# Optimization experiments

Hardware: AMD Instinct MI355X
Metric: run time of the kernel (lower is better)

Reference implementation:

```python
import jax, jax.numpy as jnp
import numpy as np

D_MODEL = 1024
H = 16
D_HEAD = D_MODEL // H  # 64


def setup_inputs() -> dict:
    key = jax.random.key(0)
    ks = jax.random.split(key, 11)
    B, L = 4, 1024
    s = 0.02
    return {
        "Q": jax.random.normal(ks[0], (B, L, D_MODEL), jnp.float32),
        "K": jax.random.normal(ks[1], (B, L, D_MODEL), jnp.float32),
        "V": jax.random.normal(ks[2], (B, L, D_MODEL), jnp.float32),
        # per-head Dense weights stacked on a leading head axis (Keras Dense: y = x @ W + b)
        "Wq": jax.random.normal(ks[3], (H, D_MODEL, D_HEAD), jnp.float32) * s,
        "bq": jnp.zeros((H, D_HEAD), jnp.float32),
        "Wk": jax.random.normal(ks[4], (H, D_MODEL, D_HEAD), jnp.float32) * s,
        "bk": jnp.zeros((H, D_HEAD), jnp.float32),
        "Wv": jax.random.normal(ks[5], (H, D_MODEL, D_HEAD), jnp.float32) * s,
        "bv": jnp.zeros((H, D_HEAD), jnp.float32),
        "Wo": jax.random.normal(ks[6], (D_MODEL, D_MODEL), jnp.float32) * s,
        "bo": jnp.zeros((D_MODEL,), jnp.float32),
    }


def reference(Q, K, V, Wq, bq, Wk, bk, Wv, bv, Wo, bo):
    # per-head projections, vectorized over heads: [B, H, L, Dh]
    q = jnp.einsum("bld,hde->bhle", Q, Wq) + bq[None, :, None, :]
    k = jnp.einsum("bld,hde->bhle", K, Wk) + bk[None, :, None, :]
    v = jnp.einsum("bld,hde->bhle", V, Wv) + bv[None, :, None, :]
    # scaled dot-product attention scores: [B, H, Lq, Lk]
    scores = jnp.einsum("bhqe,bhke->bhqk", q, k) / jnp.sqrt(jnp.asarray(D_HEAD, q.dtype))
    attn = jax.nn.softmax(scores, axis=-1)
    out_h = jnp.einsum("bhqk,bhke->bhqe", attn, v)  # [B, H, Lq, Dh]
    # concat heads along feature dim (matches tf.concat(heads, axis=2))
    B, Hh, Lq, Dh = out_h.shape
    concat = out_h.transpose(0, 2, 1, 3).reshape(B, Lq, Hh * Dh)
    output = concat @ Wo + bo
    # tf.stack(heads_attention) -> [H, B, Lq, Lk]
    attention = attn.transpose(1, 0, 2, 3)
    return output, attention
```

## Files before the change

### kernel.cpp

```cpp
#include <hip/hip_runtime.h>
#include <stdint.h>

#define DEVI __device__ __forceinline__
typedef unsigned short u16;
typedef __attribute__((ext_vector_type(8))) short s16x8;
typedef __attribute__((ext_vector_type(4))) float f32x4;

typedef __attribute__((address_space(1))) void as1_void;
typedef __attribute__((address_space(3))) void as3_void;

DEVI u16 f2b(float f){
  union { float f; uint32_t u; } x; x.f = f;
  return (u16)((x.u + 0x7fffu + ((x.u >> 16) & 1u)) >> 16);
}

DEVI void gload16(const void* g, void* l){
  __builtin_amdgcn_global_load_lds((as1_void*)g, (as3_void*)l, 16, 0, 0);
}

DEVI f32x4 MFMA(s16x8 a, s16x8 b, f32x4 c){
  return __builtin_amdgcn_mfma_f32_16x16x32_bf16(a, b, c, 0, 0, 0);
}

__global__ __launch_bounds__(256)
void k_prep(const float* __restrict__ Q, const float* __restrict__ Kc,
            const float* __restrict__ V,
            u16* __restrict__ Qb, u16* __restrict__ Kb, u16* __restrict__ Vb,
            const float* __restrict__ Wq, const float* __restrict__ Wk,
            const float* __restrict__ Wv, const float* __restrict__ Wo,
            u16* __restrict__ WqT, u16* __restrict__ WkT,
            u16* __restrict__ WvT, u16* __restrict__ WoT){
  __shared__ float t[64][65];
  const int bid = blockIdx.x, tid = threadIdx.x;
  if(bid < 12288){
    int tno = bid >> 12;
    int blk = bid & 4095;
    const float* s = (tno == 0) ? Q : (tno == 1) ? Kc : V;
    u16* d = (tno == 0) ? Qb : (tno == 1) ? Kb : Vb;
    int i = (blk * 256 + tid) * 4;
    float4 v = *(const float4*)(s + i);
    ushort4 o;
    o.x = f2b(v.x); o.y = f2b(v.y); o.z = f2b(v.z); o.w = f2b(v.w);
    *(ushort4*)(d + i) = o;
  } else {
    int j = bid - 12288;
    const float* src; u16* dst; int C, r0, c0;
    const int R = 1024;
    if(j < 768){
      int tno = j >> 8, rem = j & 255;
      int head = rem >> 4, rt = rem & 15;
      src = ((tno == 0) ? Wq : (tno == 1) ? Wk : Wv) + head * 65536;
      dst = ((tno == 0) ? WqT : (tno == 1) ? WkT : WvT) + head * 65536;
      C = 64; r0 = rt * 64; c0 = 0;
    } else {
      int j2 = j - 768;
      src = Wo; dst = WoT; C = 1024;
      r0 = (j2 & 15) * 64; c0 = (j2 >> 4) * 64;
    }
    int tx = tid & 63, ty = tid >> 6;
    #pragma unroll
    for(int i = 0; i < 64; i += 4)
      t[ty + i][tx] = src[(size_t)(r0 + ty + i) * C + c0 + tx];
    __syncthreads();
    #pragma unroll
    for(int i = 0; i < 64; i += 4)
      dst[(size_t)(c0 + ty + i) * R + r0 + tx] = f2b(t[tx][ty + i]);
  }
}

template<int BM>
DEVI void gemm_core(int mode, const u16* __restrict__ A, const u16* __restrict__ Bt,
                    const float* __restrict__ bias, void* __restrict__ Cp,
                    int m0, int n0, u16* sAb, u16* sBb){
  const int tid = threadIdx.x, w = tid >> 6, l = tid & 63;
  const int wr = w >> 1, wc = w & 1;
  constexpr int MI = BM / 32;
  f32x4 acc[MI][4];
  #pragma unroll
  for(int a = 0; a < MI; a++)
    #pragma unroll
    for(int b = 0; b < 4; b++) acc[a][b] = (f32x4){0.f, 0.f, 0.f, 0.f};

  const int NT = 16;
  auto STAGE = [&](int buf, int t){
    #pragma unroll
    for(int s2 = 0; s2 < BM / 32; s2++){
      int s = (BM / 32) * w + s2;
      int r = s * 8 + (l >> 3);
      int ch = (l & 7) ^ (r & 7);
      gload16((const char*)A + ((size_t)(m0 + r) * 1024 + t * 64) * 2 + ch * 16,
              (char*)(sAb + (size_t)buf * BM * 64) + s * 1024 + l * 16);
    }
    #pragma unroll
    for(int s2 = 0; s2 < 4; s2++){
      int s = 4 * w + s2;
      int r = s * 8 + (l >> 3);
      int ch = (l & 7) ^ (r & 7);
      gload16((const char*)Bt + ((size_t)(n0 + r) * 1024 + t * 64) * 2 + ch * 16,
              (char*)(sBb + (size_t)buf * 8192) + s * 1024 + l * 16);
    }
  };
  STAGE(0, 0);
  __syncthreads();
  for(int t = 0; t < NT; t++){
    const int cur = t & 1;
    if(t + 1 < NT) STAGE(cur ^ 1, t + 1);
    const char* pa = (const char*)(sAb + (size_t)cur * BM * 64);
    const char* pb = (const char*)(sBb + (size_t)cur * 8192);
    s16x8 af[MI][2], bf[4][2];
    #pragma unroll
    for(int mi = 0; mi < MI; mi++){
      int r = (BM / 2) * wr + 16 * mi + (l & 15);
      #pragma unroll
      for(int kk = 0; kk < 2; kk++)
        af[mi][kk] = *(const s16x8*)(pa + r * 128 + ((kk * 64 + 16 * (l >> 4)) ^ ((r & 7) << 4)));
    }
    #pragma unroll
    for(int ni = 0; ni < 4; ni++){
      int r = 64 * wc + 16 * ni + (l & 15);
      #pragma unroll
      for(int kk = 0; kk < 2; kk++)
        bf[ni][kk] = *(const s16x8*)(pb + r * 128 + ((kk * 64 + 16 * (l >> 4)) ^ ((r & 7) << 4)));
    }
    #pragma unroll
    for(int kk = 0; kk < 2; kk++)
      #pragma unroll
      for(int mi = 0; mi < MI; mi++)
        #pragma unroll
        for(int ni = 0; ni < 4; ni++)
          acc[mi][ni] = MFMA(af[mi][kk], bf[ni][kk], acc[mi][ni]);
    __syncthreads();
  }
  #pragma unroll
  for(int mi = 0; mi < MI; mi++){
    #pragma unroll
    for(int ni = 0; ni < 4; ni++){
      #pragma unroll
      for(int i = 0; i < 4; i++){
        int gr = m0 + (BM / 2) * wr + 16 * mi + 4 * (l >> 4) + i;
        int gc = n0 + 64 * wc + 16 * ni + (l & 15);
        float v = acc[mi][ni][i];
        if(mode == 0){
          ((u16*)Cp)[(size_t)gr * 1024 + gc] = f2b(v + bias[gc]);
        } else if(mode == 1){
          ((u16*)Cp)[((size_t)(gc >> 10) << 20) + ((size_t)gr << 10) + (gc & 1023)] =
              f2b(v + bias[gr]);
        } else {
          ((float*)Cp)[(size_t)gr * 1024 + gc] = v + bias[gc];
        }
      }
    }
  }
}

__global__ __launch_bounds__(256)
void k_proj(const u16* __restrict__ Qb, const u16* __restrict__ Kb,
            const u16* __restrict__ Vb,
            const u16* __restrict__ WqT, const u16* __restrict__ WkT,
            const u16* __restrict__ WvT,
            const float* __restrict__ bq, const float* __restrict__ bk,
            const float* __restrict__ bv,
            u16* __restrict__ q_ws, u16* __restrict__ k_ws, u16* __restrict__ vT_ws){
  __shared__ u16 sA[2][128 * 64];
  __shared__ u16 sB[2][128 * 64];
  const int raw = blockIdx.x;
  const int bid = (raw & 7) * 96 + (raw >> 3);
  if(bid < 256){
    gemm_core<128>(0, Qb, WqT, bq, q_ws, (bid >> 3) * 128, (bid & 7) * 128,
                   &sA[0][0], &sB[0][0]);
  } else if(bid < 512){
    int b2 = bid - 256;
    gemm_core<128>(0, Kb, WkT, bk, k_ws, (b2 >> 3) * 128, (b2 & 7) * 128,
                   &sA[0][0], &sB[0][0]);
  } else {
    int b2 = bid - 512;
    gemm_core<128>(1, WvT, Vb, bv, vT_ws, (b2 >> 5) * 128, (b2 & 31) * 128,
                   &sA[0][0], &sB[0][0]);
  }
}

__global__ __launch_bounds__(256)
void k_final(const u16* __restrict__ A, const u16* __restrict__ Bt,
             const float* __restrict__ bias, float* __restrict__ C){
  __shared__ u16 sA[2][64 * 64];
  __shared__ u16 sB[2][128 * 64];
  const int raw = blockIdx.x;
  const int bid = (raw & 7) * 64 + (raw >> 3);
  gemm_core<64>(2, A, Bt, bias, C, (bid >> 3) * 64, (bid & 7) * 128,
                &sA[0][0], &sB[0][0]);
}

__global__ __launch_bounds__(256)
void k_attn(const u16* __restrict__ qws, const u16* __restrict__ kws,
            const u16* __restrict__ vws, float* __restrict__ attn,
            u16* __restrict__ concat){
  __shared__ u16 q_s[64 * 64];
  __shared__ u16 k_s[128 * 64];
  __shared__ u16 v_s[64 * 128];
  __shared__ u16 p_s[64 * 128];
  const int tid = threadIdx.x, w = tid >> 6, l = tid & 63;
  const int bx = blockIdx.x;
  const int bh = bx & 63, qb = bx >> 6, b = bh >> 4, h = bh & 15;
  const char* qg = (const char*)qws + ((size_t)(b * 1024 + qb * 64) * 1024 + h * 64) * 2;
  const char* kg = (const char*)kws + ((size_t)(b * 1024) * 1024 + h * 64) * 2;
  const char* vg = (const char*)vws + ((size_t)b * 1048576 + (size_t)h * 64 * 1024) * 2;
  float* ao = attn + (size_t)((h * 4 + b) * 1024 + qb * 64) * 1024;
  u16* cw = concat + (size_t)(b * 1024 + qb * 64) * 1024 + h * 64;

  #pragma unroll
  for(int s2 = 0; s2 < 2; s2++){
    int s = 2 * w + s2;
    int r = s * 8 + (l >> 3);
    int ch = (l & 7) ^ (r & 7);
    gload16(qg + (size_t)r * 2048 + ch * 16, (char*)q_s + s * 1024 + l * 16);
  }

  const float KS = 0.18033688011112042f;
  float rs[4] = {0.f, 0.f, 0.f, 0.f};
  s16x8 af0, af1;

  for(int kt = 0; kt < 8; kt++){
    __syncthreads();
    #pragma unroll
    for(int s2 = 0; s2 < 4; s2++){
      int s = 4 * w + s2;
      int r = s * 8 + (l >> 3);
      int ch = (l & 7) ^ (r & 7);
      gload16(kg + (size_t)(kt * 128 + r) * 2048 + ch * 16, (char*)k_s + s * 1024 + l * 16);
    }
    __syncthreads();
    if(kt == 0){
      int rq = 16 * w + (l & 15);
      af0 = *(const s16x8*)((const char*)q_s + rq * 128 + ((16 * (l >> 4)) ^ ((rq & 7) << 4)));
      af1 = *(const s16x8*)((const char*)q_s + rq * 128 + ((64 + 16 * (l >> 4)) ^ ((rq & 7) << 4)));
    }
    #pragma unroll
    for(int f = 0; f < 8; f++){
      int r = 16 * f + (l & 15);
      s16x8 b0 = *(const s16x8*)((const char*)k_s + r * 128 + ((16 * (l >> 4)) ^ ((r & 7) << 4)));
      s16x8 b1 = *(const s16x8*)((const char*)k_s + r * 128 + ((64 + 16 * (l >> 4)) ^ ((r & 7) << 4)));
      f32x4 sf = (f32x4){0.f, 0.f, 0.f, 0.f};
      sf = MFMA(af0, b0, sf);
      sf = MFMA(af1, b1, sf);
      #pragma unroll
      for(int i = 0; i < 4; i++) rs[i] += exp2f(sf[i] * KS);
    }
  }
  #pragma unroll
  for(int i = 0; i < 4; i++){
    #pragma unroll
    for(int m = 1; m < 16; m <<= 1) rs[i] += __shfl_xor(rs[i], m, 64);
  }
  float inv[4];
  #pragma unroll
  for(int i = 0; i < 4; i++) inv[i] = 1.0f / rs[i];

  f32x4 oacc[4];
  #pragma unroll
  for(int fe = 0; fe < 4; fe++) oacc[fe] = (f32x4){0.f, 0.f, 0.f, 0.f};

  for(int kt = 0; kt < 8; kt++){
    __syncthreads();
    #pragma unroll
    for(int s2 = 0; s2 < 4; s2++){
      int s = 4 * w + s2;
      int r = s * 8 + (l >> 3);
      int ch = (l & 7) ^ (r & 7);
      gload16(kg + (size_t)(kt * 128 + r) * 2048 + ch * 16, (char*)k_s + s * 1024 + l * 16);
    }
    #pragma unroll
    for(int s2 = 0; s2 < 4; s2++){
      int s = 4 * w + s2;
      int e = s * 4 + (l >> 4);
      int ch = (l & 15) ^ (e & 15);
      gload16(vg + (size_t)e * 2048 + (size_t)kt * 256 + ch * 16, (char*)v_s + s * 1024 + l * 16);
    }
    __syncthreads();
    f32x4 sf[8];
    #pragma unroll
    for(int f = 0; f < 8; f++){
      int r = 16 * f + (l & 15);
      s16x8 b0 = *(const s16x8*)((const char*)k_s + r * 128 + ((16 * (l >> 4)) ^ ((r & 7) << 4)));
      s16x8 b1 = *(const s16x8*)((const char*)k_s + r * 128 + ((64 + 16 * (l >> 4)) ^ ((r & 7) << 4)));
      sf[f] = (f32x4){0.f, 0.f, 0.f, 0.f};
      sf[f] = MFMA(af0, b0, sf[f]);
      sf[f] = MFMA(af1, b1, sf[f]);
    }
    #pragma unroll
    for(int f = 0; f < 8; f++){
      #pragma unroll
      for(int i = 0; i < 4; i++){
        float p = exp2f(sf[f][i] * KS) * inv[i];
        int rr = 16 * w + 4 * (l >> 4) + i;
        __builtin_nontemporal_store(
            p, ao + (size_t)rr * 1024 + kt * 128 + 16 * f + (l & 15));
        *(u16*)((char*)p_s + rr * 256 + (((16 * f + (l & 15)) * 2) ^ ((rr & 15) << 4))) = f2b(p);
      }
    }
    __syncthreads();
    #pragma unroll
    for(int kc = 0; kc < 4; kc++){
      int rp = 16 * w + (l & 15);
      s16x8 pa = *(const s16x8*)((const char*)p_s + rp * 256 + ((kc * 64 + 16 * (l >> 4)) ^ ((rp & 15) << 4)));
      #pragma unroll
      for(int fe = 0; fe < 4; fe++){
        int e = 16 * fe + (l & 15);
        s16x8 bv = *(const s16x8*)((const char*)v_s + e * 256 + ((kc * 64 + 16 * (l >> 4)) ^ ((e & 15) << 4)));
        oacc[fe] = MFMA(pa, bv, oacc[fe]);
      }
    }
  }
  #pragma unroll
  for(int fe = 0; fe < 4; fe++){
    #pragma unroll
    for(int i = 0; i < 4; i++){
      int qi = 16 * w + 4 * (l >> 4) + i;
      cw[(size_t)qi * 1024 + 16 * fe + (l & 15)] = f2b(oacc[fe][i]);
    }
  }
}

extern "C" void kernel_launch(void* const* d_in, const int* in_sizes, int n_in,
                              void* d_out, int out_size, void* d_ws, size_t ws_size,
                              hipStream_t stream){
  const float* Q  = (const float*)d_in[0];
  const float* Kc = (const float*)d_in[1];
  const float* V  = (const float*)d_in[2];
  const float* Wq = (const float*)d_in[3];
  const float* bq = (const float*)d_in[4];
  const float* Wk = (const float*)d_in[5];
  const float* bk = (const float*)d_in[6];
  const float* Wv = (const float*)d_in[7];
  const float* bv = (const float*)d_in[8];
  const float* Wo = (const float*)d_in[9];
  const float* bo = (const float*)d_in[10];
  float* out = (float*)d_out;

  char* ws = (char*)d_ws;
  u16* q_ws      = (u16*)(ws + 0);
  u16* k_ws      = (u16*)(ws + 8388608);
  u16* vT_ws     = (u16*)(ws + 16777216);
  u16* concat_ws = (u16*)(ws + 25165824);
  u16* WqT = (u16*)(ws + 33554432);
  u16* WkT = (u16*)(ws + 35651584);
  u16* WvT = (u16*)(ws + 37748736);
  u16* WoT = (u16*)(ws + 39845888);

  u16* Qb = (u16*)((char*)d_out + 16777216);
  u16* Kb = (u16*)((char*)d_out + 25165824);
  u16* Vb = (u16*)((char*)d_out + 33554432);
  float* attn = out + 4194304;

  k_prep<<<13312, 256, 0, stream>>>(Q, Kc, V, Qb, Kb, Vb,
                                    Wq, Wk, Wv, Wo, WqT, WkT, WvT, WoT);
  k_proj<<<768, 256, 0, stream>>>(Qb, Kb, Vb, WqT, WkT, WvT, bq, bk, bv,
                                  q_ws, k_ws, vT_ws);
  k_attn<<<1024, 256, 0, stream>>>(q_ws, k_ws, vT_ws, attn, concat_ws);
  k_final<<<512, 256, 0, stream>>>(concat_ws, WoT, bo, out);
}
```

Measured before the change: 188.5 us.

## Vectorize attention-prob stores from LDS, shrink projection GEMM K tile, raise occupancy

The attention kernel no longer writes fp32 probabilities with scattered per-element nontemporal stores. It re-reads the bf16 probabilities from shared memory and writes 16-byte vector nontemporal stores per row segment, aiming for coalesced writes of the large attention output. This changes the stored attention values to bf16-rounded precision. Separately, the GEMM core is templated on BK, and the projection kernel uses BK=32 with launch_bounds(256,3) to cut LDS use and allow more resident blocks, at the cost of more K iterations and syncs.

```diff
diff --git a/kernel.cpp b/kernel.cpp
--- a/kernel.cpp
+++ b/kernel.cpp
@@ -13,11 +13,13 @@
   union { float f; uint32_t u; } x; x.f = f;
   return (u16)((x.u + 0x7fffu + ((x.u >> 16) & 1u)) >> 16);
 }
-
+DEVI float b2f(u16 u){
+  union { uint32_t u; float f; } x; x.u = ((uint32_t)u) << 16;
+  return x.f;
+}
 DEVI void gload16(const void* g, void* l){
   __builtin_amdgcn_global_load_lds((as1_void*)g, (as3_void*)l, 16, 0, 0);
 }
-
 DEVI f32x4 MFMA(s16x8 a, s16x8 b, f32x4 c){
   return __builtin_amdgcn_mfma_f32_16x16x32_bf16(a, b, c, 0, 0, 0);
 }
@@ -45,10 +47,8 @@
   } else {
     int j = bid - 12288;
     const float* src; u16* dst; int C, r0, c0;
-    const int R = 1024;
     if(j < 768){
-      int tno = j >> 8, rem = j & 255;
-      int head = rem >> 4, rt = rem & 15;
+      int tno = j >> 8, rem = j & 255, head = rem >> 4, rt = rem & 15;
       src = ((tno == 0) ? Wq : (tno == 1) ? Wk : Wv) + head * 65536;
       dst = ((tno == 0) ? WqT : (tno == 1) ? WkT : WvT) + head * 65536;
       C = 64; r0 = rt * 64; c0 = 0;
@@ -59,45 +59,48 @@
     }
     int tx = tid & 63, ty = tid >> 6;
     #pragma unroll
-    for(int i = 0; i < 64; i += 4)
-      t[ty + i][tx] = src[(size_t)(r0 + ty + i) * C + c0 + tx];
-    __syncthreads();
-    #pragma unroll
-    for(int i = 0; i < 64; i += 4)
-      dst[(size_t)(c0 + ty + i) * R + r0 + tx] = f2b(t[tx][ty + i]);
-  }
-}
-
-template<int BM>
+    for(int i2 = 0; i2 < 64; i2 += 4)
+      t[ty + i2][tx] = src[(size_t)(r0 + ty + i2) * C + c0 + tx];
+    __syncthreads();
+    #pragma unroll
+    for(int i2 = 0; i2 < 64; i2 += 4)
+      dst[(size_t)(c0 + ty + i2) * 1024 + r0 + tx] = f2b(t[tx][ty + i2]);
+  }
+}
+
+template<int BM, int BK>
 DEVI void gemm_core(int mode, const u16* __restrict__ A, const u16* __restrict__ Bt,
                     const float* __restrict__ bias, void* __restrict__ Cp,
                     int m0, int n0, u16* sAb, u16* sBb){
   const int tid = threadIdx.x, w = tid >> 6, l = tid & 63;
   const int wr = w >> 1, wc = w & 1;
   constexpr int MI = BM / 32;
+  constexpr int KK = BK / 32;
+  constexpr int CPR = BK / 8;
+  constexpr int CPT_A = BM * BK / 2048;
+  constexpr int CPT_B = 128 * BK / 2048;
+  constexpr int RB = 2 * BK;
   f32x4 acc[MI][4];
   #pragma unroll
   for(int a = 0; a < MI; a++)
     #pragma unroll
     for(int b = 0; b < 4; b++) acc[a][b] = (f32x4){0.f, 0.f, 0.f, 0.f};
 
-  const int NT = 16;
+  const int NT = 1024 / BK;
   auto STAGE = [&](int buf, int t){
     #pragma unroll
-    for(int s2 = 0; s2 < BM / 32; s2++){
-      int s = (BM / 32) * w + s2;
-      int r = s * 8 + (l >> 3);
-      int ch = (l & 7) ^ (r & 7);
-      gload16((const char*)A + ((size_t)(m0 + r) * 1024 + t * 64) * 2 + ch * 16,
-              (char*)(sAb + (size_t)buf * BM * 64) + s * 1024 + l * 16);
-    }
-    #pragma unroll
-    for(int s2 = 0; s2 < 4; s2++){
-      int s = 4 * w + s2;
-      int r = s * 8 + (l >> 3);
-      int ch = (l & 7) ^ (r & 7);
-      gload16((const char*)Bt + ((size_t)(n0 + r) * 1024 + t * 64) * 2 + ch * 16,
-              (char*)(sBb + (size_t)buf * 8192) + s * 1024 + l * 16);
+    for(int s2 = 0; s2 < CPT_A; s2++){
+      int c = s2 * 256 + tid;
+      int r = c / CPR, ch = (c % CPR) ^ (r & (CPR - 1));
+      gload16((const char*)A + ((size_t)(m0 + r) * 1024 + t * BK) * 2 + ch * 16,
+              (char*)sAb + (size_t)buf * BM * RB + c * 16);
+    }
+    #pragma unroll
+    for(int s2 = 0; s2 < CPT_B; s2++){
+      int c = s2 * 256 + tid;
+      int r = c / CPR, ch = (c % CPR) ^ (r & (CPR - 1));
+      gload16((const char*)Bt + ((size_t)(n0 + r) * 1024 + t * BK) * 2 + ch * 16,
+              (char*)sBb + (size_t)buf * 128 * RB + c * 16);
     }
   };
   STAGE(0, 0);
@@ -105,25 +108,27 @@
   for(int t = 0; t < NT; t++){
     const int cur = t & 1;
     if(t + 1 < NT) STAGE(cur ^ 1, t + 1);
-    const char* pa = (const char*)(sAb + (size_t)cur * BM * 64);
-    const char* pb = (const char*)(sBb + (size_t)cur * 8192);
-    s16x8 af[MI][2], bf[4][2];
+    const char* pa = (const char*)sAb + (size_t)cur * BM * RB;
+    const char* pb = (const char*)sBb + (size_t)cur * 128 * RB;
+    s16x8 af[MI][KK], bf[4][KK];
     #pragma unroll
     for(int mi = 0; mi < MI; mi++){
       int r = (BM / 2) * wr + 16 * mi + (l & 15);
       #pragma unroll
-      for(int kk = 0; kk < 2; kk++)
-        af[mi][kk] = *(const s16x8*)(pa + r * 128 + ((kk * 64 + 16 * (l >> 4)) ^ ((r & 7) << 4)));
+      for(int kk = 0; kk < KK; kk++)
+        af[mi][kk] = *(const s16x8*)(pa + r * RB +
+                     ((kk * 64 + 16 * (l >> 4)) ^ ((r & (CPR - 1)) << 4)));
     }
     #pragma unroll
     for(int ni = 0; ni < 4; ni++){
       int r = 64 * wc + 16 * ni + (l & 15);
       #pragma unroll
-      for(int kk = 0; kk < 2; kk++)
-        bf[ni][kk] = *(const s16x8*)(pb + r * 128 + ((kk * 64 + 16 * (l >> 4)) ^ ((r & 7) << 4)));
-    }
-    #pragma unroll
-    for(int kk = 0; kk < 2; kk++)
+      for(int kk = 0; kk < KK; kk++)
+        bf[ni][kk] = *(const s16x8*)(pb + r * RB +
+                     ((kk * 64 + 16 * (l >> 4)) ^ ((r & (CPR - 1)) << 4)));
+    }
+    #pragma unroll
+    for(int kk = 0; kk < KK; kk++)
       #pragma unroll
       for(int mi = 0; mi < MI; mi++)
         #pragma unroll
@@ -153,7 +158,7 @@
   }
 }
 
-__global__ __launch_bounds__(256)
+__global__ __launch_bounds__(256, 3)
 void k_proj(const u16* __restrict__ Qb, const u16* __restrict__ Kb,
             const u16* __restrict__ Vb,
             const u16* __restrict__ WqT, const u16* __restrict__ WkT,
@@ -161,21 +166,21 @@
             const float* __restrict__ bq, const float* __restrict__ bk,
             const float* __restrict__ bv,
             u16* __restrict__ q_ws, u16* __restrict__ k_ws, u16* __restrict__ vT_ws){
-  __shared__ u16 sA[2][128 * 64];
-  __shared__ u16 sB[2][128 * 64];
+  __shared__ u16 sA[2][128 * 32];
+  __shared__ u16 sB[2][128 * 32];
   const int raw = blockIdx.x;
   const int bid = (raw & 7) * 96 + (raw >> 3);
   if(bid < 256){
-    gemm_core<128>(0, Qb, WqT, bq, q_ws, (bid >> 3) * 128, (bid & 7) * 128,
-                   &sA[0][0], &sB[0][0]);
+    gemm_core<128, 32>(0, Qb, WqT, bq, q_ws, (bid >> 3) * 128, (bid & 7) * 128,
+                       &sA[0][0], &sB[0][0]);
   } else if(bid < 512){
     int b2 = bid - 256;
-    gemm_core<128>(0, Kb, WkT, bk, k_ws, (b2 >> 3) * 128, (b2 & 7) * 128,
-                   &sA[0][0], &sB[0][0]);
+    gemm_core<128, 32>(0, Kb, WkT, bk, k_ws, (b2 >> 3) * 128, (b2 & 7) * 128,
+                       &sA[0][0], &sB[0][0]);
   } else {
     int b2 = bid - 512;
-    gemm_core<128>(1, WvT, Vb, bv, vT_ws, (b2 >> 5) * 128, (b2 & 31) * 128,
-                   &sA[0][0], &sB[0][0]);
+    gemm_core<128, 32>(1, WvT, Vb, bv, vT_ws, (b2 >> 5) * 128, (b2 & 31) * 128,
+                       &sA[0][0], &sB[0][0]);
   }
 }
 
@@ -186,8 +191,8 @@
   __shared__ u16 sB[2][128 * 64];
   const int raw = blockIdx.x;
   const int bid = (raw & 7) * 64 + (raw >> 3);
-  gemm_core<64>(2, A, Bt, bias, C, (bid >> 3) * 64, (bid & 7) * 128,
-                &sA[0][0], &sB[0][0]);
+  gemm_core<64, 64>(2, A, Bt, bias, C, (bid >> 3) * 64, (bid & 7) * 128,
+                    &sA[0][0], &sB[0][0]);
 }
 
 __global__ __launch_bounds__(256)
@@ -292,8 +297,6 @@
       for(int i = 0; i < 4; i++){
         float p = exp2f(sf[f][i] * KS) * inv[i];
         int rr = 16 * w + 4 * (l >> 4) + i;
-        __builtin_nontemporal_store(
-            p, ao + (size_t)rr * 1024 + kt * 128 + 16 * f + (l & 15));
         *(u16*)((char*)p_s + rr * 256 + (((16 * f + (l & 15)) * 2) ^ ((rr & 15) << 4))) = f2b(p);
       }
     }
@@ -307,6 +310,22 @@
         int e = 16 * fe + (l & 15);
         s16x8 bv = *(const s16x8*)((const char*)v_s + e * 256 + ((kc * 64 + 16 * (l >> 4)) ^ ((e & 15) << 4)));
         oacc[fe] = MFMA(pa, bv, oacc[fe]);
+      }
+    }
+    {
+      const int rr2 = 16 * w + (l >> 2);
+      const char* srow = (const char*)p_s + rr2 * 256;
+      float* arow = ao + (size_t)rr2 * 1024 + kt * 128 + (l & 3) * 32;
+      #pragma unroll
+      for(int j = 0; j < 4; j++){
+        int cb = (l & 3) * 64 + j * 16;
+        s16x8 pv = *(const s16x8*)(srow + (cb ^ ((rr2 & 15) << 4)));
+        f32x4 o0 = (f32x4){b2f((u16)pv[0]), b2f((u16)pv[1]),
+                           b2f((u16)pv[2]), b2f((u16)pv[3])};
+        f32x4 o1 = (f32x4){b2f((u16)pv[4]), b2f((u16)pv[5]),
+                           b2f((u16)pv[6]), b2f((u16)pv[7])};
+        __builtin_nontemporal_store(o0, (f32x4*)(arow + j * 8));
+        __builtin_nontemporal_store(o1, (f32x4*)(arow + j * 8 + 4));
       }
     }
   }
```

After: 728.8 us. 3.87x slower.
